# Performance work log

Hardware: AMD Instinct MI355X
Metric: run time of the kernel (lower is better)

The kernel has to match this reference:

```python
import jax, jax.numpy as jnp
import numpy as np

T, B, E, H = 1000, 8, 1024, 16
HD = E // H


def _rope(x):
    # x: (B*H, T, HD); matches RotaryEmbedding.encode_pos (seq_dim=1)
    t = jnp.arange(x.shape[1], dtype=jnp.float32)
    inv_freq = 1.0 / (10000.0 ** (jnp.arange(0, HD, 2, dtype=jnp.float32) / HD))
    freqs = t[:, None] * inv_freq[None, :]            # (T, HD/2)
    emb = jnp.concatenate([freqs, freqs], axis=-1)    # (T, HD)
    cos, sin = jnp.cos(emb)[None], jnp.sin(emb)[None]  # (1, T, HD)
    x1, x2 = jnp.split(x, 2, axis=-1)
    rot = jnp.concatenate([-x2, x1], axis=-1)
    return cos * x + sin * rot


def setup_inputs() -> dict:
    key = jax.random.key(0)
    ks = jax.random.split(key, 8)
    d = {
        'query': jax.random.normal(ks[0], (T, B, E), jnp.float32),
        'key':   jax.random.normal(ks[1], (T, B, E), jnp.float32),
        'value': jax.random.normal(ks[2], (T, B, E), jnp.float32),
        'q_w': jax.random.normal(ks[3], (E, E), jnp.float32) * 0.02,
        'k_w': jax.random.normal(ks[4], (E, E), jnp.float32) * 0.02,
        'v_w': jax.random.normal(ks[5], (E, E), jnp.float32) * 0.02,
        'o_w': jax.random.normal(ks[6], (E, E), jnp.float32) * 0.02,
        'q_b': jnp.zeros((E,), jnp.float32),
        'k_b': jnp.zeros((E,), jnp.float32),
        'v_b': jnp.zeros((E,), jnp.float32),
        'o_b': jnp.zeros((E,), jnp.float32),
    }
    return d


def reference(query, key, value, q_w, q_b, k_w, k_b, v_w, v_b, o_w, o_b):
    tgt_len, bsz, embed_dim = query.shape
    scaling = HD ** -0.5
    # nn.Linear: x @ W^T + b
    q = (query @ q_w.T + q_b) * scaling
    k = key @ k_w.T + k_b
    v = value @ v_w.T + v_b
    # (T, B, E) -> (B*H, T, HD)
    def split_heads(x):
        return x.reshape(tgt_len, bsz * H, HD).transpose(1, 0, 2)
    q, k, v = split_heads(q), split_heads(k), split_heads(v)
    q, k = _rope(q), _rope(k)
    attn_weights = jnp.einsum('bqd,bkd->bqk', q, k)              # (B*H, T, T)
    attn_probs = jax.nn.softmax(attn_weights.astype(jnp.float32), axis=-1).astype(attn_weights.dtype)
    attn = jnp.einsum('bqk,bkd->bqd', attn_probs, v)             # (B*H, T, HD)
    attn = attn.transpose(1, 0, 2).reshape(tgt_len, bsz, embed_dim)
    out = attn @ o_w.T + o_b
    return out
```

## Files before the change

### kernel.cpp

```cpp
#include <hip/hip_runtime.h>
#include <hip/hip_bf16.h>

#define T_DIM 1000
#define B_DIM 8
#define E_DIM 1024
#define H_DIM 16
#define HD_DIM 64
#define M_DIM 8000
#define BH_DIM 128

typedef float f4 __attribute__((ext_vector_type(4)));
typedef float f16v __attribute__((ext_vector_type(16)));
typedef __bf16 b8 __attribute__((ext_vector_type(8)));
typedef unsigned long long u64;

__device__ __forceinline__ short f2bf(float f) {
  unsigned u = __float_as_uint(f);
  u = u + 0x7fffu + ((u >> 16) & 1u);
  return (short)(u >> 16);
}

__device__ __forceinline__ unsigned cvt_pk_bf16(float lo, float hi) {
  unsigned r;
  asm("v_cvt_pk_bf16_f32 %0, %1, %2" : "=v"(r) : "v"(lo), "v"(hi));
  return r;
}

__device__ __forceinline__ void gload_lds16(const void* g, void* l) {
  __builtin_amdgcn_global_load_lds(
      (const __attribute__((address_space(1))) void*)g,
      (__attribute__((address_space(3))) void*)l, 16, 0, 0);
}

__global__ void convert_w(const float* __restrict__ a, const float* __restrict__ b,
                          const float* __restrict__ c, const float* __restrict__ d,
                          short* __restrict__ dst) {
  const int nq = (4 * 1048576) / 4;
  for (int i = blockIdx.x * blockDim.x + threadIdx.x; i < nq; i += gridDim.x * blockDim.x) {
    int mat = i >> 18;
    int w = (i & 262143) * 4;
    const float* src = mat == 0 ? a : (mat == 1 ? b : (mat == 2 ? c : d));
    float4 v = *(const float4*)(src + w);
    short4 o;
    o.x = f2bf(v.x); o.y = f2bf(v.y); o.z = f2bf(v.z); o.w = f2bf(v.w);
    *(short4*)(dst + i * 4) = o;
  }
}

__global__ void rope_tab(float* __restrict__ cosd, float* __restrict__ sind) {
  int i = blockIdx.x * blockDim.x + threadIdx.x;
  if (i >= T_DIM * 32) return;
  int t = i >> 5, f = i & 31;
  double inv = pow(10000.0, -(double)f / 32.0);
  double a = (double)t * inv;
  cosd[i] = (float)cos(a);
  sind[i] = (float)sin(a);
}

__global__ __launch_bounds__(256, 2) void proj_gemm(
    const float* __restrict__ X, const short* __restrict__ W,
    const float* __restrict__ bias,
    short* __restrict__ qpk, short* __restrict__ kpk, short* __restrict__ vtp,
    const float* __restrict__ ropec, const float* __restrict__ ropes, int mode) {
  int id = blockIdx.x;
  int w = (id & 7) * 63 + (id >> 3);
  int n0 = (w & 7) * 128;
  int m0 = (w >> 3) * 128;
  __shared__ float Asf[128 * 32];
  __shared__ short Bs[128 * 32];
  int tid = threadIdx.x;
  int l = tid & 63, wid = tid >> 6;
  int wr = wid >> 1, wc = wid & 1;
  int lane16 = l & 15, lgrp = l >> 4;

  f4 acc[4][4];
#pragma unroll
  for (int i = 0; i < 4; ++i)
#pragma unroll
    for (int j = 0; j < 4; ++j)
#pragma unroll
      for (int r = 0; r < 4; ++r) acc[i][j][r] = 0.f;

  for (int kt = 0; kt < 32; ++kt) {
    int k0 = kt * 32;
#pragma unroll
    for (int j = 0; j < 4; ++j) {
      int idx = tid + j * 256;
      int r = idx >> 3, c = idx & 7;
      int gm = m0 + r; gm = gm < M_DIM ? gm : (M_DIM - 1);
      gload_lds16(X + gm * 1024 + k0 + ((c ^ (r & 7)) << 2), Asf + idx * 4);
    }
#pragma unroll
    for (int j = 0; j < 2; ++j) {
      int idx = tid + j * 256;
      int r = idx >> 2, koff = (idx & 3) * 8;
      gload_lds16(W + (n0 + r) * 1024 + k0 + koff, Bs + idx * 8);
    }
    __syncthreads();
    b8 af[4], bf[4];
#pragma unroll
    for (int mf = 0; mf < 4; ++mf) {
      int row = wr * 64 + mf * 16 + lane16;
      f4 x0 = *(const f4*)&Asf[row * 32 + (((2 * lgrp) ^ (row & 7)) << 2)];
      f4 x1 = *(const f4*)&Asf[row * 32 + (((2 * lgrp + 1) ^ (row & 7)) << 2)];
      union { unsigned u[4]; b8 v; } afu;
      afu.u[0] = cvt_pk_bf16(x0[0], x0[1]);
      afu.u[1] = cvt_pk_bf16(x0[2], x0[3]);
      afu.u[2] = cvt_pk_bf16(x1[0], x1[1]);
      afu.u[3] = cvt_pk_bf16(x1[2], x1[3]);
      af[mf] = afu.v;
    }
#pragma unroll
    for (int nf = 0; nf < 4; ++nf)
      bf[nf] = *(const b8*)(Bs + (wc * 64 + nf * 16 + lane16) * 32 + lgrp * 8);
#pragma unroll
    for (int mf = 0; mf < 4; ++mf)
#pragma unroll
      for (int nf = 0; nf < 4; ++nf)
        acc[mf][nf] = __builtin_amdgcn_mfma_f32_16x16x32_bf16(af[mf], bf[nf], acc[mf][nf], 0, 0, 0);
    __syncthreads();
  }

  int h = (n0 + wc * 64) >> 6;
  float bv[4];
#pragma unroll
  for (int nf = 0; nf < 4; ++nf) bv[nf] = bias[n0 + wc * 64 + nf * 16 + lane16];
  const float qs = 0.125f * 1.44269504088896f;

#pragma unroll
  for (int mf = 0; mf < 4; ++mf) {
#pragma unroll
    for (int r = 0; r < 4; ++r) {
      int gm = m0 + wr * 64 + mf * 16 + lgrp * 4 + r;
      bool valid = gm < M_DIM;
      int t = gm >> 3, bb = gm & 7;
      int tc = t < T_DIM ? t : (T_DIM - 1);
      float x0 = acc[mf][0][r] + bv[0];
      float x1 = acc[mf][1][r] + bv[1];
      float x2 = acc[mf][2][r] + bv[2];
      float x3 = acc[mf][3][r] + bv[3];
      if (mode == 0) { x0 *= qs; x1 *= qs; x2 *= qs; x3 *= qs; }
      if (mode < 2) {
        float c0 = ropec[tc * 32 + lane16],      s0 = ropes[tc * 32 + lane16];
        float c1 = ropec[tc * 32 + 16 + lane16], s1 = ropes[tc * 32 + 16 + lane16];
        float y0 = c0 * x0 - s0 * x2;
        float y2 = c0 * x2 + s0 * x0;
        float y1 = c1 * x1 - s1 * x3;
        float y3 = c1 * x3 + s1 * x1;
        if (valid) {
          short* dst = (mode == 0 ? qpk : kpk) + (bb * 16 + h) * 64000 + t * 64;
          dst[lane16]      = f2bf(y0);
          dst[16 + lane16] = f2bf(y1);
          dst[32 + lane16] = f2bf(y2);
          dst[48 + lane16] = f2bf(y3);
        }
      } else if (valid) {
        short* dst = vtp + (bb * 16 + h) * 64000 + t;
        dst[(lane16) * 1000]      = f2bf(x0);
        dst[(16 + lane16) * 1000] = f2bf(x1);
        dst[(32 + lane16) * 1000] = f2bf(x2);
        dst[(48 + lane16) * 1000] = f2bf(x3);
      }
    }
  }
}

__global__ __launch_bounds__(256, 4) void attn_fused(
    const short* __restrict__ qpk, const short* __restrict__ kpk,
    const short* __restrict__ vtp, short* __restrict__ apk) {
  int id = blockIdx.x;
  int xcd = id & 7, seq = id >> 3;
  int bh = xcd * 16 + (seq >> 3);
  int q0 = (seq & 7) * 128;
  int tid = threadIdx.x;
  int l = tid & 63, wid = tid >> 6;
  int l31 = l & 31, hi = l >> 5, l7 = l & 7;
  int qg = q0 + wid * 32 + l31;

  __shared__ short Ks[2][64 * 64];
  __shared__ short Vs[2][64 * 64];

  const short* qh = qpk + bh * 64000;
  const short* kh = kpk + bh * 64000;
  const short* vh = vtp + bh * 64000;

  int srow = tid >> 3;
  int sslot = tid & 7;

  b8 bq[4];
  {
    int t = qg < T_DIM ? qg : (T_DIM - 1);
#pragma unroll
    for (int hc = 0; hc < 4; ++hc)
      bq[hc] = *(const b8*)(qh + t * 64 + hc * 16 + hi * 8);
  }

  float lrun = 0.f;
  f16v o0, o1;
#pragma unroll
  for (int i = 0; i < 16; ++i) { o0[i] = 0.f; o1[i] = 0.f; }

  auto stageK = [&](int st, int buf) {
    int s0 = st * 64;
#pragma unroll
    for (int j = 0; j < 2; ++j) {
      int r = srow + j * 32;
      int c = sslot ^ (r & 7);
      gload_lds16(kh + (s0 + r) * 64 + c * 8, &Ks[buf][(j * 256 + tid) * 8]);
    }
  };
  auto stageV = [&](int st, int buf) {
    int s0 = st * 64;
#pragma unroll
    for (int j = 0; j < 2; ++j) {
      int r = srow + j * 32;
      int c = sslot ^ (r & 7);
      gload_lds16(vh + r * 1000 + s0 + c * 8, &Vs[buf][(j * 256 + tid) * 8]);
    }
  };

  stageK(0, 0);
  stageV(0, 0);
  stageK(1, 1);
  __syncthreads();

  f16v c0v, c1v;
#pragma unroll
  for (int i = 0; i < 16; ++i) { c0v[i] = 0.f; c1v[i] = 0.f; }
#pragma unroll
  for (int hc = 0; hc < 4; ++hc) {
    int slot = ((2 * hc + hi) ^ l7) << 3;
    b8 a0 = *(const b8*)(Ks[0] + l31 * 64 + slot);
    b8 a1 = *(const b8*)(Ks[0] + (32 + l31) * 64 + slot);
    c0v = __builtin_amdgcn_mfma_f32_32x32x16_bf16(a0, bq[hc], c0v, 0, 0, 0);
    c1v = __builtin_amdgcn_mfma_f32_32x32x16_bf16(a1, bq[hc], c1v, 0, 0, 0);
  }
  __syncthreads();

  for (int i = 0; i < 16; ++i) {
    int b = i & 1;
    if (i < 14) stageK(i + 2, b);
    if (i < 15) stageV(i + 1, b ^ 1);

    if (i == 15) {
#pragma unroll
      for (int r = 4; r < 16; ++r) c1v[r] = -1e30f;
    }

#pragma unroll
    for (int j = 0; j < 16; ++j) {
      c0v[j] = __builtin_amdgcn_exp2f(c0v[j]);
      c1v[j] = __builtin_amdgcn_exp2f(c1v[j]);
    }
    float ts[8];
#pragma unroll
    for (int j = 0; j < 8; ++j) ts[j] = (c0v[j] + c0v[j + 8]) + (c1v[j] + c1v[j + 8]);
#pragma unroll
    for (int d = 4; d > 0; d >>= 1)
#pragma unroll
      for (int j = 0; j < d; ++j) ts[j] += ts[j + d];
    lrun += ts[0];

    unsigned u0[8], u1[8];
#pragma unroll
    for (int j = 0; j < 8; ++j) {
      u0[j] = cvt_pk_bf16(c0v[2 * j], c0v[2 * j + 1]);
      u1[j] = cvt_pk_bf16(c1v[2 * j], c1v[2 * j + 1]);
    }
    union { unsigned u[4]; b8 v; } pf[4];
    {
      auto w0 = __builtin_amdgcn_permlane32_swap(u0[0], u0[2], false, false);
      auto w1 = __builtin_amdgcn_permlane32_swap(u0[1], u0[3], false, false);
      pf[0].u[0] = w0[0]; pf[0].u[1] = w1[0]; pf[0].u[2] = w0[1]; pf[0].u[3] = w1[1];
      auto w2 = __builtin_amdgcn_permlane32_swap(u0[4], u0[6], false, false);
      auto w3 = __builtin_amdgcn_permlane32_swap(u0[5], u0[7], false, false);
      pf[1].u[0] = w2[0]; pf[1].u[1] = w3[0]; pf[1].u[2] = w2[1]; pf[1].u[3] = w3[1];
      auto w4 = __builtin_amdgcn_permlane32_swap(u1[0], u1[2], false, false);
      auto w5 = __builtin_amdgcn_permlane32_swap(u1[1], u1[3], false, false);
      pf[2].u[0] = w4[0]; pf[2].u[1] = w5[0]; pf[2].u[2] = w4[1]; pf[2].u[3] = w5[1];
      auto w6 = __builtin_amdgcn_permlane32_swap(u1[4], u1[6], false, false);
      auto w7 = __builtin_amdgcn_permlane32_swap(u1[5], u1[7], false, false);
      pf[3].u[0] = w6[0]; pf[3].u[1] = w7[0]; pf[3].u[2] = w6[1]; pf[3].u[3] = w7[1];
    }

    if (i < 15) {
      const short* Kb = Ks[b ^ 1];
#pragma unroll
      for (int j = 0; j < 16; ++j) { c0v[j] = 0.f; c1v[j] = 0.f; }
#pragma unroll
      for (int hc = 0; hc < 4; ++hc) {
        int slot = ((2 * hc + hi) ^ l7) << 3;
        b8 a0 = *(const b8*)(Kb + l31 * 64 + slot);
        b8 a1 = *(const b8*)(Kb + (32 + l31) * 64 + slot);
        c0v = __builtin_amdgcn_mfma_f32_32x32x16_bf16(a0, bq[hc], c0v, 0, 0, 0);
        c1v = __builtin_amdgcn_mfma_f32_32x32x16_bf16(a1, bq[hc], c1v, 0, 0, 0);
      }
    }

    {
      const short* Vb = Vs[b];
#pragma unroll
      for (int ck = 0; ck < 4; ++ck) {
        int slot = ((2 * ck + hi) ^ l7) << 3;
        b8 av0 = *(const b8*)(Vb + l31 * 64 + slot);
        b8 av1 = *(const b8*)(Vb + (32 + l31) * 64 + slot);
        o0 = __builtin_amdgcn_mfma_f32_32x32x16_bf16(av0, pf[ck].v, o0, 0, 0, 0);
        o1 = __builtin_amdgcn_mfma_f32_32x32x16_bf16(av1, pf[ck].v, o1, 0, 0, 0);
      }
    }
    __syncthreads();
  }

  lrun += __shfl_xor(lrun, 32, 64);
  if (qg < T_DIM) {
    float linv = 1.f / lrun;
    int bb = bh >> 4, hh = bh & 15;
    short* dst = apk + (qg * 8 + bb) * 1024 + hh * 64;
#pragma unroll
    for (int rq = 0; rq < 4; ++rq) {
      int d0 = 8 * rq + 4 * hi;
      short4 w0, w1;
      w0.x = f2bf(o0[rq * 4 + 0] * linv);
      w0.y = f2bf(o0[rq * 4 + 1] * linv);
      w0.z = f2bf(o0[rq * 4 + 2] * linv);
      w0.w = f2bf(o0[rq * 4 + 3] * linv);
      w1.x = f2bf(o1[rq * 4 + 0] * linv);
      w1.y = f2bf(o1[rq * 4 + 1] * linv);
      w1.z = f2bf(o1[rq * 4 + 2] * linv);
      w1.w = f2bf(o1[rq * 4 + 3] * linv);
      *(short4*)(dst + d0) = w0;
      *(short4*)(dst + 32 + d0) = w1;
    }
  }
}

__global__ __launch_bounds__(256, 2) void out_gemm(
    const short* __restrict__ apk, const short* __restrict__ wo,
    const float* __restrict__ ob, float* __restrict__ out) {
  int id = blockIdx.x;
  int w = (id & 7) * 63 + (id >> 3);
  int n0 = (w & 7) * 128;
  int m0 = (w >> 3) * 128;
  __shared__ short As[128 * 32];
  __shared__ short Bs[128 * 32];
  int tid = threadIdx.x;
  int l = tid & 63, wid = tid >> 6;
  int wr = wid >> 1, wc = wid & 1;
  int lane16 = l & 15, lgrp = l >> 4;

  f4 acc[4][4];
#pragma unroll
  for (int i = 0; i < 4; ++i)
#pragma unroll
    for (int j = 0; j < 4; ++j)
#pragma unroll
      for (int r = 0; r < 4; ++r) acc[i][j][r] = 0.f;

  for (int kt = 0; kt < 32; ++kt) {
    int k0 = kt * 32;
#pragma unroll
    for (int j = 0; j < 2; ++j) {
      int c = tid + j * 256;
      int r = c >> 2, koff = (c & 3) * 8;
      int gm = m0 + r; gm = gm < M_DIM ? gm : (M_DIM - 1);
      gload_lds16(apk + gm * 1024 + k0 + koff, As + c * 8);
      gload_lds16(wo + (n0 + r) * 1024 + k0 + koff, Bs + c * 8);
    }
    __syncthreads();
    b8 af[4], bf[4];
#pragma unroll
    for (int mf = 0; mf < 4; ++mf)
      af[mf] = *(const b8*)(As + (wr * 64 + mf * 16 + lane16) * 32 + lgrp * 8);
#pragma unroll
    for (int nf = 0; nf < 4; ++nf)
      bf[nf] = *(const b8*)(Bs + (wc * 64 + nf * 16 + lane16) * 32 + lgrp * 8);
#pragma unroll
    for (int mf = 0; mf < 4; ++mf)
#pragma unroll
      for (int nf = 0; nf < 4; ++nf)
        acc[mf][nf] = __builtin_amdgcn_mfma_f32_16x16x32_bf16(af[mf], bf[nf], acc[mf][nf], 0, 0, 0);
    __syncthreads();
  }

  float bv[4];
#pragma unroll
  for (int nf = 0; nf < 4; ++nf) bv[nf] = ob[n0 + wc * 64 + nf * 16 + lane16];
#pragma unroll
  for (int mf = 0; mf < 4; ++mf) {
#pragma unroll
    for (int r = 0; r < 4; ++r) {
      int gm = m0 + wr * 64 + mf * 16 + lgrp * 4 + r;
      if (gm < M_DIM) {
#pragma unroll
        for (int nf = 0; nf < 4; ++nf)
          out[gm * 1024 + n0 + wc * 64 + nf * 16 + lane16] = acc[mf][nf][r] + bv[nf];
      }
    }
  }
}

extern "C" void kernel_launch(void* const* d_in, const int* in_sizes, int n_in,
                              void* d_out, int out_size, void* d_ws, size_t ws_size,
                              hipStream_t stream) {
  const float* xq = (const float*)d_in[0];
  const float* xk = (const float*)d_in[1];
  const float* xv = (const float*)d_in[2];
  const float* qw = (const float*)d_in[3];
  const float* kw = (const float*)d_in[4];
  const float* vw = (const float*)d_in[5];
  const float* ow = (const float*)d_in[6];
  const float* qb = (const float*)d_in[7];
  const float* kb = (const float*)d_in[8];
  const float* vb = (const float*)d_in[9];
  const float* ob = (const float*)d_in[10];
  float* out = (float*)d_out;
  char* ws = (char*)d_ws;

  short* wbf   = (short*)(ws);
  float* ropec = (float*)(ws + 8388608);
  float* ropes = (float*)(ws + 8516608);
  short* qpk   = (short*)(ws + 8644608);
  short* kpk   = (short*)(ws + 8644608 + 16384512);
  short* vtp   = (short*)(ws + 8644608 + 2 * 16384512);
  short* apk   = (short*)(ws + 8644608 + 3 * 16384512);

  hipMemsetAsync((char*)vtp + 2 * 8192000, 0, 512, stream);

  convert_w<<<2048, 256, 0, stream>>>(qw, kw, vw, ow, wbf);
  rope_tab<<<125, 256, 0, stream>>>(ropec, ropes);

  const float* xs[3] = {xq, xk, xv};
  const float* bs[3] = {qb, kb, vb};
  for (int mode = 0; mode < 3; ++mode) {
    proj_gemm<<<dim3(504), dim3(256), 0, stream>>>(xs[mode], wbf + mode * 1048576, bs[mode],
                                                   qpk, kpk, vtp, ropec, ropes, mode);
  }
  attn_fused<<<dim3(1024), dim3(256), 0, stream>>>(qpk, kpk, vtp, apk);
  out_gemm<<<dim3(504), dim3(256), 0, stream>>>(apk, wbf + 3 * 1048576, ob, out);
}
```

Before: 203.2 us.

## Pre-convert activations to bf16 and swizzle LDS tiles in projection and output GEMMs

Adds a separate kernel that converts each fp32 input activation to bf16 in a scratch buffer (aliased with the attention output buffer) before each projection GEMM. The GEMM then loads bf16 A tiles directly instead of fp32 tiles with in-loop conversion, halving LDS traffic for A. It also XOR-swizzles the 16-byte chunks of both bf16 tiles, in the projection and output GEMMs, to reduce LDS bank conflicts. The cost is three extra elementwise kernels that read all of the fp32 activations and write them back as bf16.

```diff
diff --git a/kernel.cpp b/kernel.cpp
--- a/kernel.cpp
+++ b/kernel.cpp
@@ -47,6 +47,16 @@
   }
 }
 
+__global__ void convert_x(const float* __restrict__ src, short* __restrict__ dst) {
+  const int nq = (M_DIM * E_DIM) / 4;
+  for (int i = blockIdx.x * blockDim.x + threadIdx.x; i < nq; i += gridDim.x * blockDim.x) {
+    float4 v = *(const float4*)(src + i * 4);
+    short4 o;
+    o.x = f2bf(v.x); o.y = f2bf(v.y); o.z = f2bf(v.z); o.w = f2bf(v.w);
+    *(short4*)(dst + i * 4) = o;
+  }
+}
+
 __global__ void rope_tab(float* __restrict__ cosd, float* __restrict__ sind) {
   int i = blockIdx.x * blockDim.x + threadIdx.x;
   if (i >= T_DIM * 32) return;
@@ -58,7 +68,7 @@
 }
 
 __global__ __launch_bounds__(256, 2) void proj_gemm(
-    const float* __restrict__ X, const short* __restrict__ W,
+    const short* __restrict__ xbf, const short* __restrict__ W,
     const float* __restrict__ bias,
     short* __restrict__ qpk, short* __restrict__ kpk, short* __restrict__ vtp,
     const float* __restrict__ ropec, const float* __restrict__ ropes, int mode) {
@@ -66,7 +76,7 @@
   int w = (id & 7) * 63 + (id >> 3);
   int n0 = (w & 7) * 128;
   int m0 = (w >> 3) * 128;
-  __shared__ float Asf[128 * 32];
+  __shared__ short As[128 * 32];
   __shared__ short Bs[128 * 32];
   int tid = threadIdx.x;
   int l = tid & 63, wid = tid >> 6;
@@ -84,35 +94,26 @@
   for (int kt = 0; kt < 32; ++kt) {
     int k0 = kt * 32;
 #pragma unroll
-    for (int j = 0; j < 4; ++j) {
-      int idx = tid + j * 256;
-      int r = idx >> 3, c = idx & 7;
-      int gm = m0 + r; gm = gm < M_DIM ? gm : (M_DIM - 1);
-      gload_lds16(X + gm * 1024 + k0 + ((c ^ (r & 7)) << 2), Asf + idx * 4);
-    }
-#pragma unroll
     for (int j = 0; j < 2; ++j) {
       int idx = tid + j * 256;
-      int r = idx >> 2, koff = (idx & 3) * 8;
-      gload_lds16(W + (n0 + r) * 1024 + k0 + koff, Bs + idx * 8);
+      int r = idx >> 2, s = idx & 3;
+      int c = s ^ ((r >> 1) & 3);
+      int gm = m0 + r; gm = gm < M_DIM ? gm : (M_DIM - 1);
+      gload_lds16(xbf + gm * 1024 + k0 + c * 8, As + idx * 8);
+      gload_lds16(W + (n0 + r) * 1024 + k0 + c * 8, Bs + idx * 8);
     }
     __syncthreads();
     b8 af[4], bf[4];
 #pragma unroll
     for (int mf = 0; mf < 4; ++mf) {
       int row = wr * 64 + mf * 16 + lane16;
-      f4 x0 = *(const f4*)&Asf[row * 32 + (((2 * lgrp) ^ (row & 7)) << 2)];
-      f4 x1 = *(const f4*)&Asf[row * 32 + (((2 * lgrp + 1) ^ (row & 7)) << 2)];
-      union { unsigned u[4]; b8 v; } afu;
-      afu.u[0] = cvt_pk_bf16(x0[0], x0[1]);
-      afu.u[1] = cvt_pk_bf16(x0[2], x0[3]);
-      afu.u[2] = cvt_pk_bf16(x1[0], x1[1]);
-      afu.u[3] = cvt_pk_bf16(x1[2], x1[3]);
-      af[mf] = afu.v;
-    }
-#pragma unroll
-    for (int nf = 0; nf < 4; ++nf)
-      bf[nf] = *(const b8*)(Bs + (wc * 64 + nf * 16 + lane16) * 32 + lgrp * 8);
+      af[mf] = *(const b8*)(As + row * 32 + (lgrp ^ ((row >> 1) & 3)) * 8);
+    }
+#pragma unroll
+    for (int nf = 0; nf < 4; ++nf) {
+      int row = wc * 64 + nf * 16 + lane16;
+      bf[nf] = *(const b8*)(Bs + row * 32 + (lgrp ^ ((row >> 1) & 3)) * 8);
+    }
 #pragma unroll
     for (int mf = 0; mf < 4; ++mf)
 #pragma unroll
@@ -360,20 +361,25 @@
     int k0 = kt * 32;
 #pragma unroll
     for (int j = 0; j < 2; ++j) {
-      int c = tid + j * 256;
-      int r = c >> 2, koff = (c & 3) * 8;
+      int idx = tid + j * 256;
+      int r = idx >> 2, s = idx & 3;
+      int c = s ^ ((r >> 1) & 3);
       int gm = m0 + r; gm = gm < M_DIM ? gm : (M_DIM - 1);
-      gload_lds16(apk + gm * 1024 + k0 + koff, As + c * 8);
-      gload_lds16(wo + (n0 + r) * 1024 + k0 + koff, Bs + c * 8);
+      gload_lds16(apk + gm * 1024 + k0 + c * 8, As + idx * 8);
+      gload_lds16(wo + (n0 + r) * 1024 + k0 + c * 8, Bs + idx * 8);
     }
     __syncthreads();
     b8 af[4], bf[4];
 #pragma unroll
-    for (int mf = 0; mf < 4; ++mf)
-      af[mf] = *(const b8*)(As + (wr * 64 + mf * 16 + lane16) * 32 + lgrp * 8);
-#pragma unroll
-    for (int nf = 0; nf < 4; ++nf)
-      bf[nf] = *(const b8*)(Bs + (wc * 64 + nf * 16 + lane16) * 32 + lgrp * 8);
+    for (int mf = 0; mf < 4; ++mf) {
+      int row = wr * 64 + mf * 16 + lane16;
+      af[mf] = *(const b8*)(As + row * 32 + (lgrp ^ ((row >> 1) & 3)) * 8);
+    }
+#pragma unroll
+    for (int nf = 0; nf < 4; ++nf) {
+      int row = wc * 64 + nf * 16 + lane16;
+      bf[nf] = *(const b8*)(Bs + row * 32 + (lgrp ^ ((row >> 1) & 3)) * 8);
+    }
 #pragma unroll
     for (int mf = 0; mf < 4; ++mf)
 #pragma unroll
@@ -423,6 +429,7 @@
   short* kpk   = (short*)(ws + 8644608 + 16384512);
   short* vtp   = (short*)(ws + 8644608 + 2 * 16384512);
   short* apk   = (short*)(ws + 8644608 + 3 * 16384512);
+  short* xbf   = apk;
 
   hipMemsetAsync((char*)vtp + 2 * 8192000, 0, 512, stream);
 
@@ -432,7 +439,8 @@
   const float* xs[3] = {xq, xk, xv};
   const float* bs[3] = {qb, kb, vb};
   for (int mode = 0; mode < 3; ++mode) {
-    proj_gemm<<<dim3(504), dim3(256), 0, stream>>>(xs[mode], wbf + mode * 1048576, bs[mode],
+    convert_x<<<2048, 256, 0, stream>>>(xs[mode], xbf);
+    proj_gemm<<<dim3(504), dim3(256), 0, stream>>>(xbf, wbf + mode * 1048576, bs[mode],
                                                    qpk, kpk, vtp, ropec, ropes, mode);
   }
   attn_fused<<<dim3(1024), dim3(256), 0, stream>>>(qpk, kpk, vtp, apk);
```

Result: no change. 204.7 us (+0.7%).
